# Optimization experiments

Hardware: AMD Instinct MI355X
Metric: run time of the kernel (lower is better)

Reference implementation:

```python
import jax, jax.numpy as jnp
import numpy as np

N, E, H = 50000, 800000, 128
LN_EPS = 1e-5  # torch nn.LayerNorm default


def layer_norm(x, gamma, beta):
    mu = jnp.mean(x, axis=-1, keepdims=True)
    var = jnp.mean((x - mu) ** 2, axis=-1, keepdims=True)
    return (x - mu) * jax.lax.rsqrt(var + LN_EPS) * gamma + beta


def setup_inputs() -> dict:
    key = jax.random.key(0)
    ks = jax.random.split(key, 8)
    sc = 1.0 / np.sqrt(2 * H)
    return {
        "x": jax.random.normal(ks[0], (N, H), dtype=jnp.float32),
        "edge_index": jax.random.randint(ks[1], (2, E), 0, N, dtype=jnp.int64),
        "edge_weights": jax.random.uniform(ks[2], (E,), dtype=jnp.float32),
        "msg_w": jax.random.normal(ks[3], (2 * H, H), dtype=jnp.float32) * sc,
        "msg_b": jnp.zeros((H,), jnp.float32),
        "msg_g": jnp.ones((H,), jnp.float32),
        "msg_beta": jnp.zeros((H,), jnp.float32),
        "upd_w": jax.random.normal(ks[4], (2 * H, H), dtype=jnp.float32) * sc,
        "upd_b": jnp.zeros((H,), jnp.float32),
        "upd_g": jnp.ones((H,), jnp.float32),
        "upd_beta": jnp.zeros((H,), jnp.float32),
        "gate_w": jax.random.normal(ks[5], (H, 1), dtype=jnp.float32) / np.sqrt(H),
        "gate_b": jnp.zeros((1,), jnp.float32),
    }


def reference(x, edge_index, edge_weights, msg_w, msg_b, msg_g, msg_beta,
              upd_w, upd_b, upd_g, upd_beta, gate_w, gate_b):
    num_nodes = x.shape[0]
    src, dst = edge_index[0], edge_index[1]
    # per-edge gather -> MLP -> weighted message  [E, H]
    em = jnp.concatenate([x[src], x[dst]], axis=-1)          # [E, 2H]
    em = jax.nn.relu(layer_norm(em @ msg_w + msg_b, msg_g, msg_beta))
    em = em * edge_weights[:, None]
    # scatter-add to destination nodes + mean normalization
    msgs = jax.ops.segment_sum(em, dst, num_segments=num_nodes)           # [N, H]
    counts = jax.ops.segment_sum(jnp.ones((src.shape[0], 1), x.dtype), dst,
                                 num_segments=num_nodes)                  # [N, 1]
    valid = (counts > 0).astype(x.dtype)
    messages = msgs / (counts + 1e-8) * valid
    # gated update
    gate = jax.nn.sigmoid(x @ gate_w + gate_b)                            # [N, 1]
    combined = jnp.concatenate([x, messages], axis=-1)                    # [N, 2H]
    h_new = jax.nn.relu(layer_norm(combined @ upd_w + upd_b, upd_g, upd_beta))
    return gate * h_new + (1.0 - gate) * x
```

## Files before the change

### kernel.cpp

```cpp
#include <hip/hip_runtime.h>
#include <math.h>

#define H 128
#define LN_EPS 1e-5f

typedef __attribute__((ext_vector_type(8))) short  bf16x8;
typedef __attribute__((ext_vector_type(4))) float  f32x4;
typedef __attribute__((ext_vector_type(8))) unsigned short ushort8v;

__device__ __forceinline__ int imin(int a, int b) { return a < b ? a : b; }
__device__ __forceinline__ int clampi(int v, int lo, int hi) { return v < lo ? lo : (v > hi ? hi : v); }
__device__ __forceinline__ unsigned short f2bf(float f) {
    unsigned u = __float_as_uint(f);
    unsigned r = (u + 0x7fffu + ((u >> 16) & 1u)) >> 16;
    return (unsigned short)r;
}
__device__ __forceinline__ float bf2f(unsigned short u) {
    return __uint_as_float(((unsigned)u) << 16);
}

__global__ void count_kernel(const int* __restrict__ dst, int* __restrict__ cnt, int E, int n) {
    int i = blockIdx.x * blockDim.x + threadIdx.x;
    int e = i * 4;
    if (e + 3 < E) {
        int4 d4 = *(const int4*)(dst + e);
        atomicAdd(&cnt[clampi(d4.x, 0, n - 1)], 1);
        atomicAdd(&cnt[clampi(d4.y, 0, n - 1)], 1);
        atomicAdd(&cnt[clampi(d4.z, 0, n - 1)], 1);
        atomicAdd(&cnt[clampi(d4.w, 0, n - 1)], 1);
    } else {
        for (; e < E; ++e) atomicAdd(&cnt[clampi(dst[e], 0, n - 1)], 1);
    }
}

__global__ __launch_bounds__(256) void scan1_kernel(const int* __restrict__ cnt,
                                                    int* __restrict__ cursor,
                                                    int* __restrict__ bsum, int n) {
    __shared__ int wsum[4];
    const int tid = threadIdx.x, lane = tid & 63, wv = tid >> 6;
    int idx = blockIdx.x * 256 + tid;
    int v = (idx < n) ? cnt[idx] : 0;
    int s = v;
    #pragma unroll
    for (int off = 1; off < 64; off <<= 1) {
        int u = __shfl_up(s, off);
        if (lane >= off) s += u;
    }
    if (lane == 63) wsum[wv] = s;
    __syncthreads();
    int add = 0;
    for (int i = 0; i < wv; ++i) add += wsum[i];
    int incl = s + add;
    if (idx < n) cursor[idx] = incl - v;
    if (tid == 255) bsum[blockIdx.x] = incl;
}

__global__ __launch_bounds__(256) void scan2_kernel(int* __restrict__ bsum, int nb) {
    __shared__ int wsum[4];
    const int tid = threadIdx.x, lane = tid & 63, wv = tid >> 6;
    int carry = 0;
    for (int base = 0; base < nb; base += 256) {
        int idx = base + tid;
        int v = (idx < nb) ? bsum[idx] : 0;
        int s = v;
        #pragma unroll
        for (int off = 1; off < 64; off <<= 1) {
            int u = __shfl_up(s, off);
            if (lane >= off) s += u;
        }
        if (lane == 63) wsum[wv] = s;
        __syncthreads();
        int add = 0;
        for (int i = 0; i < wv; ++i) add += wsum[i];
        if (idx < nb) bsum[idx] = s + add + carry - v;
        int tot = wsum[0] + wsum[1] + wsum[2] + wsum[3];
        __syncthreads();
        carry += tot;
    }
}

__global__ void cvt_weights(const float* __restrict__ msg_w, const float* __restrict__ upd_w,
                            unsigned short* __restrict__ wtT, unsigned short* __restrict__ wbT,
                            unsigned short* __restrict__ wuT) {
    int tid = blockIdx.x * blockDim.x + threadIdx.x;
    int m = tid >> 14;
    int r = tid & 16383;
    int d = r >> 7, k = r & 127;
    float v;
    unsigned short* dstp;
    if (m == 0)      { v = msg_w[k * 128 + d];          dstp = wtT; }
    else if (m == 1) { v = msg_w[(128 + k) * 128 + d];  dstp = wbT; }
    else if (m == 2) { v = upd_w[k * 128 + d];          dstp = wuT; }
    else             { v = upd_w[(128 + k) * 128 + d];  dstp = wuT + 16384; }
    dstp[d * 128 + k] = f2bf(v);
}

__global__ __launch_bounds__(256) void pre_both_mfma(
    const float* __restrict__ x,
    const unsigned short* __restrict__ wtT, const unsigned short* __restrict__ wbT,
    const float* __restrict__ bias, unsigned short* __restrict__ xb,
    unsigned short* __restrict__ tsrcb, unsigned short* __restrict__ tdstb,
    float* __restrict__ saRow, float* __restrict__ stRow, int n,
    const int* __restrict__ src, const int* __restrict__ dst,
    const float* __restrict__ ew, int* __restrict__ cursor,
    const int* __restrict__ boff, unsigned long long* __restrict__ swP,
    int E, int epb)
{
    __shared__ unsigned short Wt[16384];
    __shared__ unsigned short Wb[16384];
    const int tid = threadIdx.x, lane = tid & 63, wv = tid >> 6;
    const int dbase = lane & 15, kgrp = lane >> 4;
    const int swzl = (dbase & 7) << 4;
    const int r0 = blockIdx.x * 64;

    {
        const ushort8v* st = (const ushort8v*)wtT;
        const ushort8v* sb = (const ushort8v*)wbT;
        for (int c = tid; c < 2048; c += 256) {
            int d = c >> 4, slot = c & 15;
            int off = d * 256 + ((slot * 16) ^ ((d & 7) << 4));
            *(ushort8v*)((char*)Wt + off) = st[c];
            *(ushort8v*)((char*)Wb + off) = sb[c];
        }
    }

    int rowA = imin(r0 + wv * 16 + dbase, n - 1);
    bf16x8 a[4];
    {
        const float* xr = x + (size_t)rowA * H + kgrp * 8;
        #pragma unroll
        for (int s = 0; s < 4; ++s) {
            float4 f0 = *(const float4*)(xr + s * 32);
            float4 f1 = *(const float4*)(xr + s * 32 + 4);
            bf16x8 v;
            v[0] = (short)f2bf(f0.x); v[1] = (short)f2bf(f0.y);
            v[2] = (short)f2bf(f0.z); v[3] = (short)f2bf(f0.w);
            v[4] = (short)f2bf(f1.x); v[5] = (short)f2bf(f1.y);
            v[6] = (short)f2bf(f1.z); v[7] = (short)f2bf(f1.w);
            a[s] = v;
            *(bf16x8*)(xb + (size_t)rowA * H + s * 32 + kgrp * 8) = v;
        }
    }
    __syncthreads();

    f32x4 accT[8], accB[8];
    #pragma unroll
    for (int t = 0; t < 8; ++t) { accT[t] = (f32x4){0.f,0.f,0.f,0.f}; accB[t] = (f32x4){0.f,0.f,0.f,0.f}; }
    #pragma unroll
    for (int s = 0; s < 4; ++s) {
        #pragma unroll
        for (int t = 0; t < 8; ++t) {
            int off = (t * 16 + dbase) * 256 + ((s * 64 + kgrp * 16) ^ swzl);
            bf16x8 bt = *(const bf16x8*)((const char*)Wt + off);
            bf16x8 bb = *(const bf16x8*)((const char*)Wb + off);
            accT[t] = __builtin_amdgcn_mfma_f32_16x16x32_bf16(a[s], bt, accT[t], 0, 0, 0);
            accB[t] = __builtin_amdgcn_mfma_f32_16x16x32_bf16(a[s], bb, accB[t], 0, 0, 0);
        }
    }

    float ub[8];
    #pragma unroll
    for (int t = 0; t < 8; ++t) ub[t] = bias[t * 16 + dbase];
    #pragma unroll
    for (int r = 0; r < 4; ++r) {
        int row = r0 + wv * 16 + kgrp * 4 + r;
        if (row < n) {
            unsigned short sv[8], tv[8];
            float sa = 0.f, st = 0.f;
            #pragma unroll
            for (int t = 0; t < 8; ++t) {
                unsigned short av = f2bf(accT[t][r]);
                unsigned short dv = f2bf(accB[t][r] + ub[t]);
                sv[t] = av; tv[t] = dv;
                sa += bf2f(av); st += bf2f(dv);
            }
            #pragma unroll
            for (int t = 0; t < 8; ++t) {
                tsrcb[(size_t)row * H + t * 16 + dbase] = sv[t];
                tdstb[(size_t)row * H + t * 16 + dbase] = tv[t];
            }
            sa += __shfl_xor(sa, 1); st += __shfl_xor(st, 1);
            sa += __shfl_xor(sa, 2); st += __shfl_xor(st, 2);
            sa += __shfl_xor(sa, 4); st += __shfl_xor(st, 4);
            sa += __shfl_xor(sa, 8); st += __shfl_xor(st, 8);
            if (dbase == 0) { saRow[row] = sa; stRow[row] = st; }
        }
    }

    {
        const int ebase = blockIdx.x * epb;
        const int eend  = imin(ebase + epb, E);
        for (int e = ebase + tid; e < eend; e += 1024) {
            int dd[4]; unsigned long long vv[4]; int pp[4];
            int m = 0;
            #pragma unroll
            for (int u = 0; u < 4; ++u) {
                int ec = e + u * 256;
                if (ec < eend) {
                    int d = clampi(dst[ec], 0, n - 1);
                    int s = clampi(src[ec], 0, n - 1);
                    vv[m] = ((unsigned long long)__float_as_uint(ew[ec]) << 32) | (unsigned)s;
                    dd[m] = d;
                    ++m;
                }
            }
            #pragma unroll
            for (int u = 0; u < 4; ++u)
                if (u < m) pp[u] = atomicAdd(&cursor[dd[u]], 1) + boff[dd[u] >> 8];
            #pragma unroll
            for (int u = 0; u < 4; ++u)
                if (u < m) swP[pp[u]] = vv[u];
        }
    }
}

__global__ __launch_bounds__(256) void node_msg_kernel(
    const unsigned short* __restrict__ tsrcb,
    const unsigned short* __restrict__ tdstb,
    const float* __restrict__ saRow, const float* __restrict__ stRow,
    const unsigned long long* __restrict__ swP,
    const int* __restrict__ cnt, const int* __restrict__ endoff,
    const int* __restrict__ boff,
    const float* __restrict__ gamma, const float* __restrict__ beta,
    unsigned short* __restrict__ msgsb, int n)
{
    const int tid  = threadIdx.x;
    const int lane = tid & 63;
    const int qq   = lane & 15;
    const int node = blockIdx.x * 16 + (tid >> 4);
    if (node >= n) return;
    const int k   = cnt[node];
    const int e0  = endoff[node] + boff[node >> 8] - k;

    float td[8];
    {
        ushort8v t = *(const ushort8v*)(tdstb + (size_t)node * H + qq * 8);
        #pragma unroll
        for (int j = 0; j < 8; ++j) td[j] = bf2f((unsigned short)t[j]);
    }
    const float St = stRow[node];
    float g_[8], b_[8];
    #pragma unroll
    for (int j = 0; j < 8; ++j) { g_[j] = gamma[qq * 8 + j]; b_[j] = beta[qq * 8 + j]; }

    float acc[8];
    #pragma unroll
    for (int j = 0; j < 8; ++j) acc[j] = 0.f;

    ushort8v A0 = {}, A1 = {};
    float W0 = 0.f, W1 = 0.f, S0 = 0.f, S1 = 0.f;
    if (k > 0) {
        unsigned long long sw = swP[e0];
        int s = (int)(unsigned)sw; W0 = __uint_as_float((unsigned)(sw >> 32));
        S0 = saRow[s]; A0 = *(const ushort8v*)(tsrcb + (size_t)s * H + qq * 8);
    }
    if (k > 1) {
        unsigned long long sw = swP[e0 + 1];
        int s = (int)(unsigned)sw; W1 = __uint_as_float((unsigned)(sw >> 32));
        S1 = saRow[s]; A1 = *(const ushort8v*)(tsrcb + (size_t)s * H + qq * 8);
    }

    for (int i = 0; i < k; i += 2) {
        ushort8v A2 = {}, A3 = {};
        float W2 = 0.f, W3 = 0.f, S2 = 0.f, S3 = 0.f;
        if (i + 2 < k) {
            unsigned long long sw = swP[e0 + i + 2];
            int s = (int)(unsigned)sw; W2 = __uint_as_float((unsigned)(sw >> 32));
            S2 = saRow[s]; A2 = *(const ushort8v*)(tsrcb + (size_t)s * H + qq * 8);
        }
        if (i + 3 < k) {
            unsigned long long sw = swP[e0 + i + 3];
            int s = (int)(unsigned)sw; W3 = __uint_as_float((unsigned)(sw >> 32));
            S3 = saRow[s]; A3 = *(const ushort8v*)(tsrcb + (size_t)s * H + qq * 8);
        }

        float v0[8], v1[8];
        float sq0 = 0.f, sq1 = 0.f;
        #pragma unroll
        for (int j = 0; j < 8; ++j) {
            v0[j] = td[j] + bf2f((unsigned short)A0[j]);
            sq0 = fmaf(v0[j], v0[j], sq0);
        }
        #pragma unroll
        for (int j = 0; j < 8; ++j) {
            v1[j] = td[j] + bf2f((unsigned short)A1[j]);
            sq1 = fmaf(v1[j], v1[j], sq1);
        }
        sq0 += __shfl_xor(sq0, 1); sq1 += __shfl_xor(sq1, 1);
        sq0 += __shfl_xor(sq0, 2); sq1 += __shfl_xor(sq1, 2);
        sq0 += __shfl_xor(sq0, 4); sq1 += __shfl_xor(sq1, 4);
        sq0 += __shfl_xor(sq0, 8); sq1 += __shfl_xor(sq1, 8);

        {
            float mu  = (S0 + St) * (1.f / 128.f);
            float var = sq0 * (1.f / 128.f) - mu * mu;
            float ri  = rsqrtf(fmaxf(var, 0.f) + LN_EPS);
            float nmr = -mu * ri;
            #pragma unroll
            for (int j = 0; j < 8; ++j) {
                float t = fmaf(v0[j], ri, nmr);
                float val = fmaf(t, g_[j], b_[j]);
                acc[j] = fmaf(fmaxf(val, 0.f), W0, acc[j]);
            }
        }
        {
            float mu  = (S1 + St) * (1.f / 128.f);
            float var = sq1 * (1.f / 128.f) - mu * mu;
            float ri  = rsqrtf(fmaxf(var, 0.f) + LN_EPS);
            float nmr = -mu * ri;
            #pragma unroll
            for (int j = 0; j < 8; ++j) {
                float t = fmaf(v1[j], ri, nmr);
                float val = fmaf(t, g_[j], b_[j]);
                acc[j] = fmaf(fmaxf(val, 0.f), W1, acc[j]);
            }
        }
        A0 = A2; W0 = W2; S0 = S2;
        A1 = A3; W1 = W3; S1 = S3;
    }

    float scale = (k > 0) ? 1.f / ((float)k + 1e-8f) : 0.f;
    ushort8v o;
    #pragma unroll
    for (int j = 0; j < 8; ++j) o[j] = f2bf(acc[j] * scale);
    *(ushort8v*)(msgsb + (size_t)node * H + qq * 8) = o;
}

__global__ __launch_bounds__(256) void update_mfma(
    const unsigned short* __restrict__ xb,
    const unsigned short* __restrict__ msgsb,
    const unsigned short* __restrict__ wuT,
    const float* __restrict__ upd_b, const float* __restrict__ g,
    const float* __restrict__ beta, const float* __restrict__ gate_w,
    const float* __restrict__ gate_b, float* __restrict__ out, int n)
{
    __shared__ unsigned short W2[2][16384];
    const int tid = threadIdx.x, lane = tid & 63, wv = tid >> 6;
    const int dbase = lane & 15, kgrp = lane >> 4;
    const int swzl = (dbase & 7) << 4;
    const int r0 = blockIdx.x * 64;

    {
        const ushort8v* srcp = (const ushort8v*)wuT;
        for (int c = tid; c < 4096; c += 256) {
            int m = c >> 11, c2 = c & 2047;
            int d = c2 >> 4, slot = c2 & 15;
            int off = m * 32768 + d * 256 + ((slot * 16) ^ ((d & 7) << 4));
            *(ushort8v*)((char*)W2 + off) = srcp[c];
        }
    }

    int rowA = imin(r0 + wv * 16 + dbase, n - 1);
    bf16x8 ax[4], am[4];
    {
        const char* arow = (const char*)(xb + (size_t)rowA * H) + kgrp * 16;
        const char* mrow = (const char*)(msgsb + (size_t)rowA * H) + kgrp * 16;
        #pragma unroll
        for (int s = 0; s < 4; ++s) {
            ax[s] = *(const bf16x8*)(arow + s * 64);
            am[s] = *(const bf16x8*)(mrow + s * 64);
        }
    }
    __syncthreads();

    f32x4 acc[8];
    #pragma unroll
    for (int t = 0; t < 8; ++t) acc[t] = (f32x4){0.f, 0.f, 0.f, 0.f};
    #pragma unroll
    for (int s = 0; s < 4; ++s) {
        #pragma unroll
        for (int t = 0; t < 8; ++t) {
            int off = (t * 16 + dbase) * 256 + ((s * 64 + kgrp * 16) ^ swzl);
            bf16x8 b = *(const bf16x8*)((const char*)W2 + off);
            acc[t] = __builtin_amdgcn_mfma_f32_16x16x32_bf16(ax[s], b, acc[t], 0, 0, 0);
        }
    }
    #pragma unroll
    for (int s = 0; s < 4; ++s) {
        #pragma unroll
        for (int t = 0; t < 8; ++t) {
            int off = 32768 + (t * 16 + dbase) * 256 + ((s * 64 + kgrp * 16) ^ swzl);
            bf16x8 b = *(const bf16x8*)((const char*)W2 + off);
            acc[t] = __builtin_amdgcn_mfma_f32_16x16x32_bf16(am[s], b, acc[t], 0, 0, 0);
        }
    }

    float ub[8], g_[8], be_[8], gw_[8];
    #pragma unroll
    for (int t = 0; t < 8; ++t) {
        int d = t * 16 + dbase;
        ub[t] = upd_b[d]; g_[t] = g[d]; be_[t] = beta[d]; gw_[t] = gate_w[d];
    }
    const float gb = gate_b[0];

    #pragma unroll
    for (int r = 0; r < 4; ++r) {
        int row = r0 + wv * 16 + kgrp * 4 + r;
        if (row >= n) continue;
        const unsigned short* xr = xb + (size_t)row * H + dbase;
        float xf[8], v[8];
        float sum = 0.f, sq = 0.f, gs = 0.f;
        #pragma unroll
        for (int t = 0; t < 8; ++t) {
            xf[t] = bf2f(xr[t * 16]);
            float val = acc[t][r] + ub[t];
            v[t] = val;
            sum += val;
            sq = fmaf(val, val, sq);
            gs = fmaf(xf[t], gw_[t], gs);
        }
        sum += __shfl_xor(sum, 1); sq += __shfl_xor(sq, 1); gs += __shfl_xor(gs, 1);
        sum += __shfl_xor(sum, 2); sq += __shfl_xor(sq, 2); gs += __shfl_xor(gs, 2);
        sum += __shfl_xor(sum, 4); sq += __shfl_xor(sq, 4); gs += __shfl_xor(gs, 4);
        sum += __shfl_xor(sum, 8); sq += __shfl_xor(sq, 8); gs += __shfl_xor(gs, 8);
        float mu  = sum * (1.f / 128.f);
        float var = sq * (1.f / 128.f) - mu * mu;
        float ri  = rsqrtf(fmaxf(var, 0.f) + LN_EPS);
        float gate = 1.f / (1.f + expf(-(gs + gb)));
        float* orow = out + (size_t)row * H + dbase;
        #pragma unroll
        for (int t = 0; t < 8; ++t) {
            float h = fmaf((v[t] - mu) * ri, g_[t], be_[t]);
            h = fmaxf(h, 0.f);
            orow[t * 16] = fmaf(gate, h - xf[t], xf[t]);
        }
    }
}

extern "C" void kernel_launch(void* const* d_in, const int* in_sizes, int n_in,
                              void* d_out, int out_size, void* d_ws, size_t ws_size,
                              hipStream_t stream)
{
    const float* x        = (const float*)d_in[0];
    const int*   ei       = (const int*)d_in[1];
    const float* ew       = (const float*)d_in[2];
    const float* msg_w    = (const float*)d_in[3];
    const float* msg_b    = (const float*)d_in[4];
    const float* msg_g    = (const float*)d_in[5];
    const float* msg_beta = (const float*)d_in[6];
    const float* upd_w    = (const float*)d_in[7];
    const float* upd_b    = (const float*)d_in[8];
    const float* upd_g    = (const float*)d_in[9];
    const float* upd_beta = (const float*)d_in[10];
    const float* gate_w   = (const float*)d_in[11];
    const float* gate_b   = (const float*)d_in[12];

    const int n = in_sizes[0] / H;
    const int E = in_sizes[2];
    const int* src = ei;
    const int* dst = ei + E;

    char* p = (char*)d_ws;
    auto alloc = [&](size_t bytes) { char* r = p; p += (bytes + 255) & ~(size_t)255; return r; };
    int*   cnt    = (int*)alloc((size_t)n * 4);
    int*   cursor = (int*)alloc((size_t)n * 4);
    int*   bsum   = (int*)alloc((size_t)1024 * 4);
    unsigned long long* swP = (unsigned long long*)alloc((size_t)E * 8);
    float* saRow  = (float*)alloc((size_t)n * 4);
    float* stRow  = (float*)alloc((size_t)n * 4);
    unsigned short* xb    = (unsigned short*)alloc((size_t)n * H * 2);
    unsigned short* tsrcb = (unsigned short*)alloc((size_t)n * H * 2);
    unsigned short* tdstb = (unsigned short*)alloc((size_t)n * H * 2);
    unsigned short* msgsb = (unsigned short*)alloc((size_t)n * H * 2);
    unsigned short* wtT   = (unsigned short*)alloc((size_t)H * H * 2);
    unsigned short* wbT   = (unsigned short*)alloc((size_t)H * H * 2);
    unsigned short* wuT   = (unsigned short*)alloc((size_t)2 * H * H * 2);

    hipMemsetAsync(cnt, 0, (size_t)n * 4, stream);

    const int nb = (n + 255) / 256;
    int eb4 = ((E + 3) / 4 + 255) / 256;
    count_kernel<<<eb4, 256, 0, stream>>>(dst, cnt, E, n);
    scan1_kernel<<<nb, 256, 0, stream>>>(cnt, cursor, bsum, n);
    scan2_kernel<<<1, 256, 0, stream>>>(bsum, nb);

    cvt_weights<<<256, 256, 0, stream>>>(msg_w, upd_w, wtT, wbT, wuT);

    const int nblocks = (n + 63) / 64;
    const int epb = (E + nblocks - 1) / nblocks;
    pre_both_mfma<<<nblocks, 256, 0, stream>>>(x, wtT, wbT, msg_b, xb, tsrcb, tdstb,
                                               saRow, stRow, n,
                                               src, dst, ew, cursor, bsum, swP, E, epb);

    node_msg_kernel<<<(n + 15) / 16, 256, 0, stream>>>(tsrcb, tdstb, saRow, stRow, swP,
                                                       cnt, cursor, bsum,
                                                       msg_g, msg_beta, msgsb, n);

    update_mfma<<<(n + 63) / 64, 256, 0, stream>>>(xb, msgsb, wuT, upd_b, upd_g, upd_beta,
                                                   gate_w, gate_b, (float*)d_out, n);
}
```

Baseline: 184.6 us.

## Split edge CSR scatter into coarse block-bucket pass and fine LDS-ranked pass

Replaces per-node global atomic cursors in the edge scatter with a two-level bucketing. First, edges go into 256-node buckets using per-bucket global atomics. Then a new kernel places each edge at its final slot using shared-memory atomics per node. The aim is less global atomic contention and more locality in the scattered writes. The cost is an extra E*8-byte buffer, one more read/write pass over the edges and an extra kernel launch. Source indices are packed into 16 bits, which silently assumes n <= 65536.

Result: slower. 597.5 us (+223.8%).

```diff
diff --git a/kernel.cpp b/kernel.cpp
--- a/kernel.cpp
+++ b/kernel.cpp
@@ -34,7 +34,7 @@
 }
 
 __global__ __launch_bounds__(256) void scan1_kernel(const int* __restrict__ cnt,
-                                                    int* __restrict__ cursor,
+                                                    int* __restrict__ curScan,
                                                     int* __restrict__ bsum, int n) {
     __shared__ int wsum[4];
     const int tid = threadIdx.x, lane = tid & 63, wv = tid >> 6;
@@ -51,7 +51,7 @@
     int add = 0;
     for (int i = 0; i < wv; ++i) add += wsum[i];
     int incl = s + add;
-    if (idx < n) cursor[idx] = incl - v;
+    if (idx < n) curScan[idx] = incl - v;
     if (tid == 255) bsum[blockIdx.x] = incl;
 }
 
@@ -102,8 +102,8 @@
     unsigned short* __restrict__ tsrcb, unsigned short* __restrict__ tdstb,
     float* __restrict__ saRow, float* __restrict__ stRow, int n,
     const int* __restrict__ src, const int* __restrict__ dst,
-    const float* __restrict__ ew, int* __restrict__ cursor,
-    const int* __restrict__ boff, unsigned long long* __restrict__ swP,
+    const float* __restrict__ ew, int* __restrict__ bcur,
+    const int* __restrict__ bbase, unsigned long long* __restrict__ coarse,
     int E, int epb)
 {
     __shared__ unsigned short Wt[16384];
@@ -199,18 +199,42 @@
                 if (ec < eend) {
                     int d = clampi(dst[ec], 0, n - 1);
                     int s = clampi(src[ec], 0, n - 1);
-                    vv[m] = ((unsigned long long)__float_as_uint(ew[ec]) << 32) | (unsigned)s;
-                    dd[m] = d;
+                    vv[m] = ((unsigned long long)__float_as_uint(ew[ec]) << 32)
+                          | ((unsigned)(d & 255) << 16) | (unsigned)(s & 0xFFFF);
+                    dd[m] = d >> 8;
                     ++m;
                 }
             }
             #pragma unroll
             for (int u = 0; u < 4; ++u)
-                if (u < m) pp[u] = atomicAdd(&cursor[dd[u]], 1) + boff[dd[u] >> 8];
+                if (u < m) pp[u] = atomicAdd(&bcur[dd[u]], 1) + bbase[dd[u]];
             #pragma unroll
             for (int u = 0; u < 4; ++u)
-                if (u < m) swP[pp[u]] = vv[u];
-        }
+                if (u < m) coarse[pp[u]] = vv[u];
+        }
+    }
+}
+
+__global__ __launch_bounds__(256) void scatter_fine(
+    const unsigned long long* __restrict__ coarse,
+    const int* __restrict__ bbase, const int* __restrict__ curScan,
+    unsigned long long* __restrict__ swP, int nb, int n, int E)
+{
+    __shared__ int rank[256];
+    __shared__ int cbase[256];
+    const int b = blockIdx.x;
+    const int base = bbase[b];
+    const int end  = (b + 1 < nb) ? bbase[b + 1] : E;
+    const int nodebase = b << 8;
+    rank[threadIdx.x] = 0;
+    cbase[threadIdx.x] = (nodebase + threadIdx.x < n) ? curScan[nodebase + threadIdx.x] : 0;
+    __syncthreads();
+    for (int i = base + threadIdx.x; i < end; i += 256) {
+        unsigned long long v = coarse[i];
+        int dl = (int)((v >> 16) & 255);
+        int r = atomicAdd(&rank[dl], 1);
+        int p = base + cbase[dl] + r;
+        swP[p] = (v & 0xFFFFFFFF00000000ull) | (v & 0xFFFFull);
     }
 }
 
@@ -219,8 +243,8 @@
     const unsigned short* __restrict__ tdstb,
     const float* __restrict__ saRow, const float* __restrict__ stRow,
     const unsigned long long* __restrict__ swP,
-    const int* __restrict__ cnt, const int* __restrict__ endoff,
-    const int* __restrict__ boff,
+    const int* __restrict__ cnt, const int* __restrict__ curScan,
+    const int* __restrict__ bbase,
     const float* __restrict__ gamma, const float* __restrict__ beta,
     unsigned short* __restrict__ msgsb, int n)
 {
@@ -229,8 +253,8 @@
     const int qq   = lane & 15;
     const int node = blockIdx.x * 16 + (tid >> 4);
     if (node >= n) return;
-    const int k   = cnt[node];
-    const int e0  = endoff[node] + boff[node >> 8] - k;
+    const int k  = cnt[node];
+    const int e0 = bbase[node >> 8] + curScan[node];
 
     float td[8];
     {
@@ -452,10 +476,12 @@
 
     char* p = (char*)d_ws;
     auto alloc = [&](size_t bytes) { char* r = p; p += (bytes + 255) & ~(size_t)255; return r; };
-    int*   cnt    = (int*)alloc((size_t)n * 4);
-    int*   cursor = (int*)alloc((size_t)n * 4);
-    int*   bsum   = (int*)alloc((size_t)1024 * 4);
-    unsigned long long* swP = (unsigned long long*)alloc((size_t)E * 8);
+    int*   cnt     = (int*)alloc((size_t)n * 4);
+    int*   curScan = (int*)alloc((size_t)n * 4);
+    int*   bsum    = (int*)alloc((size_t)1024 * 4);
+    int*   bcur    = (int*)alloc((size_t)1024 * 4);
+    unsigned long long* coarse = (unsigned long long*)alloc((size_t)E * 8);
+    unsigned long long* swP    = (unsigned long long*)alloc((size_t)E * 8);
     float* saRow  = (float*)alloc((size_t)n * 4);
     float* stRow  = (float*)alloc((size_t)n * 4);
     unsigned short* xb    = (unsigned short*)alloc((size_t)n * H * 2);
@@ -467,11 +493,12 @@
     unsigned short* wuT   = (unsigned short*)alloc((size_t)2 * H * H * 2);
 
     hipMemsetAsync(cnt, 0, (size_t)n * 4, stream);
+    hipMemsetAsync(bcur, 0, (size_t)1024 * 4, stream);
 
     const int nb = (n + 255) / 256;
     int eb4 = ((E + 3) / 4 + 255) / 256;
     count_kernel<<<eb4, 256, 0, stream>>>(dst, cnt, E, n);
-    scan1_kernel<<<nb, 256, 0, stream>>>(cnt, cursor, bsum, n);
+    scan1_kernel<<<nb, 256, 0, stream>>>(cnt, curScan, bsum, n);
     scan2_kernel<<<1, 256, 0, stream>>>(bsum, nb);
 
     cvt_weights<<<256, 256, 0, stream>>>(msg_w, upd_w, wtT, wbT, wuT);
@@ -480,10 +507,12 @@
     const int epb = (E + nblocks - 1) / nblocks;
     pre_both_mfma<<<nblocks, 256, 0, stream>>>(x, wtT, wbT, msg_b, xb, tsrcb, tdstb,
                                                saRow, stRow, n,
-                                               src, dst, ew, cursor, bsum, swP, E, epb);
+                                               src, dst, ew, bcur, bsum, coarse, E, epb);
+
+    scatter_fine<<<nb, 256, 0, stream>>>(coarse, bsum, curScan, swP, nb, n, E);
 
     node_msg_kernel<<<(n + 15) / 16, 256, 0, stream>>>(tsrcb, tdstb, saRow, stRow, swP,
-                                                       cnt, cursor, bsum,
+                                                       cnt, curScan, bsum,
                                                        msg_g, msg_beta, msgsb, n);
 
     update_mfma<<<(n + 63) / 64, 256, 0, stream>>>(xb, msgsb, wuT, upd_b, upd_g, upd_beta,
```
